# Optimization experiments

Hardware: AMD Instinct MI355X
Metric: run time of the kernel (lower is better)

The kernel has to match this reference:

```python
import jax, jax.numpy as jnp
import numpy as np

B, T, IN = 32, 1024, 256
H = 128          # hidden_size
NL = 2           # num_layers
NC = 4           # num_classes
F2 = 2 * H       # bidirectional feature size


def _lstm_dir(xs, w_ih, w_hh, b_ih, b_hh, reverse):
    # xs: [T, B, in]; w_ih: [4H, in]; w_hh: [4H, H]
    if reverse:
        xs = xs[::-1]
    h0 = jnp.zeros((xs.shape[1], H), xs.dtype)
    c0 = jnp.zeros((xs.shape[1], H), xs.dtype)

    def step(carry, xt):
        h, c = carry
        g = xt @ w_ih.T + b_ih + h @ w_hh.T + b_hh  # [B, 4H]
        i, f, gg, o = jnp.split(g, 4, axis=-1)       # PyTorch gate order i,f,g,o
        c = jax.nn.sigmoid(f) * c + jax.nn.sigmoid(i) * jnp.tanh(gg)
        h = jax.nn.sigmoid(o) * jnp.tanh(c)
        return (h, c), h

    _, hs = jax.lax.scan(step, (h0, c0), xs)  # [T, B, H]
    if reverse:
        hs = hs[::-1]
    return hs


def setup_inputs() -> dict:
    key = jax.random.key(0)
    ks = jax.random.split(key, 12)
    s = 0.05
    x = jax.random.normal(ks[0], (B, T, IN), jnp.float32)
    # stacked LSTM params: [layer, direction, ...]; layer0 in = IN, layer1 in = 2H = IN
    w_ih = jax.random.normal(ks[1], (NL, 2, 4 * H, IN), jnp.float32) * s
    w_hh = jax.random.normal(ks[2], (NL, 2, 4 * H, H), jnp.float32) * s
    b_ih = jax.random.normal(ks[3], (NL, 2, 4 * H), jnp.float32) * s
    b_hh = jax.random.normal(ks[4], (NL, 2, 4 * H), jnp.float32) * s
    wq = jax.random.normal(ks[5], (F2, F2), jnp.float32) * s
    wk = jax.random.normal(ks[6], (F2, F2), jnp.float32) * s
    wv = jax.random.normal(ks[7], (F2, F2), jnp.float32) * s
    bq = jax.random.normal(ks[8], (F2,), jnp.float32) * s
    bk = jax.random.normal(ks[9], (F2,), jnp.float32) * s
    bv = jax.random.normal(ks[10], (F2,), jnp.float32) * s
    w_fc = jax.random.normal(ks[11], (NC, F2), jnp.float32) * s
    b_fc = jnp.zeros((NC,), jnp.float32)
    return {"x": x, "w_ih": w_ih, "w_hh": w_hh, "b_ih": b_ih, "b_hh": b_hh,
            "wq": wq, "wk": wk, "wv": wv, "bq": bq, "bk": bk, "bv": bv,
            "w_fc": w_fc, "b_fc": b_fc}


def reference(x, w_ih, w_hh, b_ih, b_hh, wq, wk, wv, bq, bk, bv, w_fc, b_fc):
    # --- biLSTM (eval mode: inter-layer dropout inactive) ---
    xs = jnp.swapaxes(x, 0, 1)  # time-major [T, B, IN]
    for l in range(NL):
        fwd = _lstm_dir(xs, w_ih[l, 0], w_hh[l, 0], b_ih[l, 0], b_hh[l, 0], False)
        bwd = _lstm_dir(xs, w_ih[l, 1], w_hh[l, 1], b_ih[l, 1], b_hh[l, 1], True)
        xs = jnp.concatenate([fwd, bwd], axis=-1)  # [T, B, 2H]
    out = jnp.swapaxes(xs, 0, 1)  # [B, T, 2H]
    # --- naive full self-attention ---
    q = out @ wq.T + bq
    k = out @ wk.T + bk
    v = out @ wv.T + bv
    scores = jnp.einsum('btd,bsd->bts', q, k) / jnp.sqrt(jnp.float32(F2))
    attn = jax.nn.softmax(scores, axis=-1)          # [B, T, T]
    ctx = jnp.einsum('bts,bsd->btd', attn, v)       # [B, T, 2H]
    # --- FC head on last timestep ---
    return ctx[:, -1, :] @ w_fc.T + b_fc            # [B, NC]
```

## Files before the change

### kernel.cpp

```cpp
#include <hip/hip_runtime.h>
#include <math.h>
#include <stdint.h>

#define BB 32
#define TT 1024
#define HH 128
#define G4 512
#define CH 16

typedef _Float16 half2_t __attribute__((ext_vector_type(2)));
typedef _Float16 half8_t __attribute__((ext_vector_type(8)));
typedef float f32x4 __attribute__((ext_vector_type(4)));

__device__ __forceinline__ float fdot2f(half2_t a, half2_t b, float c) {
    return __builtin_amdgcn_fdot2(a, b, c, false);
}
__device__ __forceinline__ float rcpf(float x) {
    return __builtin_amdgcn_rcpf(x);
}
__device__ __forceinline__ float dpp_xor1(float x) {
    return __builtin_bit_cast(float, __builtin_amdgcn_update_dpp(
        0, __builtin_bit_cast(int, x), 0xB1, 0xF, 0xF, true));
}
__device__ __forceinline__ float dpp_xor2(float x) {
    return __builtin_bit_cast(float, __builtin_amdgcn_update_dpp(
        0, __builtin_bit_cast(int, x), 0x4E, 0xF, 0xF, true));
}
__device__ __forceinline__ void bar_lgkm() {
    asm volatile("s_waitcnt lgkmcnt(0)\n\ts_barrier" ::: "memory");
}

__global__ __launch_bounds__(256) void cvt_wih(
    const float* __restrict__ w, _Float16* __restrict__ o)
{
    const int i = (blockIdx.x * 256 + threadIdx.x) * 4;
    float4 f = *(const float4*)(w + i);
    half2_t t[2] = { half2_t{(_Float16)f.x, (_Float16)f.y},
                     half2_t{(_Float16)f.z, (_Float16)f.w} };
    *(float2*)(o + i) = *(float2*)t;
}

__global__ __launch_bounds__(512, 1) void lstm_fused(
    const float* __restrict__ x_in,
    const _Float16* __restrict__ wih16_l,
    const float* __restrict__ b_ih_l,
    const float* __restrict__ b_hh_l,
    const float* __restrict__ w_hh_l,
    float* __restrict__ out)
{
    const int b = blockIdx.x & 31;
    const int d = blockIdx.x >> 5;
    const int tid = threadIdx.x;
    const int wvid = tid >> 6;
    const int l = tid & 63;
    const int s = l & 3;
    const int g = l >> 2;
    const int j = (wvid << 4) | g;

    __shared__ __align__(16) _Float16 hs[HH];
    __shared__ __align__(16) float xp[2][CH * 512];
    __shared__ __align__(16) half2_t xr[2][CH * 128];
    __shared__ __align__(16) float obuf[CH * HH];

    half2_t wv[4][16];
#pragma unroll
    for (int G = 0; G < 4; ++G) {
        const float* wr = w_hh_l + (size_t)(d * G4 + 128 * G + j) * HH + 32 * s;
#pragma unroll
        for (int q4 = 0; q4 < 8; ++q4) {
            float4 f = *(const float4*)(wr + 4 * q4);
            wv[G][2 * q4]     = half2_t{(_Float16)f.x, (_Float16)f.y};
            wv[G][2 * q4 + 1] = half2_t{(_Float16)f.z, (_Float16)f.w};
        }
    }

    const int acol0 = wvid * 64 + (l & 15);
    const _Float16* wn = wih16_l + ((size_t)d * G4 + acol0) * 256 + (l >> 4) * 8;
    const float bias0 = b_ih_l[d * G4 + acol0]      + b_hh_l[d * G4 + acol0];
    const float bias1 = b_ih_l[d * G4 + acol0 + 16] + b_hh_l[d * G4 + acol0 + 16];
    const float bias2 = b_ih_l[d * G4 + acol0 + 32] + b_hh_l[d * G4 + acol0 + 32];
    const float bias3 = b_ih_l[d * G4 + acol0 + 48] + b_hh_l[d * G4 + acol0 + 48];

    const float* xbase = x_in + (size_t)b * TT * 256;

    const int a_noswz = (l & 15) * 512 + (l >> 4) * 16;
    const int a_swz   = (l & 7) << 4;
    const int w_swz_byte = (tid * 16) ^ (((tid >> 5) & 7) << 4);

#pragma unroll 1
    for (int p = 0; p < 2; ++p) {
        const int tlo = d ? (1008 - p * CH) : p * CH;
        const float* gs = xbase + (size_t)tlo * 256 + tid * 8;
        float4 f0 = *(const float4*)gs;
        float4 f1 = *(const float4*)(gs + 4);
        half2_t t4[4] = { half2_t{(_Float16)f0.x, (_Float16)f0.y},
                          half2_t{(_Float16)f0.z, (_Float16)f0.w},
                          half2_t{(_Float16)f1.x, (_Float16)f1.y},
                          half2_t{(_Float16)f1.z, (_Float16)f1.w} };
        *(float4*)((char*)xr[p] + w_swz_byte) = *(float4*)t4;
    }
    __syncthreads();

    f32x4 acc0 = {bias0, bias0, bias0, bias0};
    f32x4 acc1 = {bias1, bias1, bias1, bias1};
    f32x4 acc2 = {bias2, bias2, bias2, bias2};
    f32x4 acc3 = {bias3, bias3, bias3, bias3};

#pragma unroll
    for (int kt = 0; kt < 8; ++kt) {
        half8_t af = *(const half8_t*)((const char*)xr[0] + ((a_noswz + kt * 64) ^ a_swz));
        acc0 = __builtin_amdgcn_mfma_f32_16x16x32_f16(af, *(const half8_t*)(wn +         kt * 32), acc0, 0, 0, 0);
        acc1 = __builtin_amdgcn_mfma_f32_16x16x32_f16(af, *(const half8_t*)(wn +  4096 + kt * 32), acc1, 0, 0, 0);
        acc2 = __builtin_amdgcn_mfma_f32_16x16x32_f16(af, *(const half8_t*)(wn +  8192 + kt * 32), acc2, 0, 0, 0);
        acc3 = __builtin_amdgcn_mfma_f32_16x16x32_f16(af, *(const half8_t*)(wn + 12288 + kt * 32), acc3, 0, 0, 0);
    }
    {
        const int rb = (l >> 4) * 4;
#pragma unroll
        for (int q = 0; q < 4; ++q) {
            xp[0][(rb + q) * 512 + acol0]      = acc0[q];
            xp[0][(rb + q) * 512 + acol0 + 16] = acc1[q];
            xp[0][(rb + q) * 512 + acol0 + 32] = acc2[q];
            xp[0][(rb + q) * 512 + acol0 + 48] = acc3[q];
        }
    }
    acc0 = (f32x4){bias0, bias0, bias0, bias0};
    acc1 = (f32x4){bias1, bias1, bias1, bias1};
    acc2 = (f32x4){bias2, bias2, bias2, bias2};
    acc3 = (f32x4){bias3, bias3, bias3, bias3};

    if (tid < 64) ((half2_t*)hs)[tid] = half2_t{(_Float16)0.f, (_Float16)0.f};
    float c = 0.f;
    float* ob = out + (size_t)b * TT * 256 + d * HH;
    __syncthreads();

    float4 rg0 = {}, rg1 = {};
    half8_t afrag = {};
    for (int ck = 0; ck < 64; ++ck) {
        const int cur = ck & 1;
        const bool doproj = (ck + 1 < 64);
        if (ck + 2 < 64) {
            const int tlo2 = d ? (1008 - (ck + 2) * CH) : (ck + 2) * CH;
            const float* gs = xbase + (size_t)tlo2 * 256 + tid * 8;
            rg0 = *(const float4*)gs;
            rg1 = *(const float4*)(gs + 4);
        }
        const float* xb = xp[cur];
        const char* xr_rd = (const char*)xr[cur ^ 1];

#pragma unroll 1
        for (int si = 0; si < CH; ++si) {
            half8_t bA = {}, bB = {};
            if (doproj) {
                const int kt = si >> 1;
                if (!(si & 1)) {
                    afrag = *(const half8_t*)(xr_rd + ((a_noswz + kt * 64) ^ a_swz));
                    bA = *(const half8_t*)(wn +        kt * 32);
                    bB = *(const half8_t*)(wn + 4096 + kt * 32);
                } else {
                    bA = *(const half8_t*)(wn +  8192 + kt * 32);
                    bB = *(const half8_t*)(wn + 12288 + kt * 32);
                }
            }

            const int lds_t = d ? (CH - 1 - si) : si;

            const float xi = xb[lds_t * 512 +       j];
            const float xf = xb[lds_t * 512 + 128 + j];
            const float xg = xb[lds_t * 512 + 256 + j];
            const float xo = xb[lds_t * 512 + 384 + j];

            const float4* hp = (const float4*)(hs + 32 * s);
            float4 hA = hp[0], hB = hp[1], hC = hp[2], hD = hp[3];
            half2_t hh[16];
            hh[0]  = __builtin_bit_cast(half2_t, hA.x);
            hh[1]  = __builtin_bit_cast(half2_t, hA.y);
            hh[2]  = __builtin_bit_cast(half2_t, hA.z);
            hh[3]  = __builtin_bit_cast(half2_t, hA.w);
            hh[4]  = __builtin_bit_cast(half2_t, hB.x);
            hh[5]  = __builtin_bit_cast(half2_t, hB.y);
            hh[6]  = __builtin_bit_cast(half2_t, hB.z);
            hh[7]  = __builtin_bit_cast(half2_t, hB.w);
            hh[8]  = __builtin_bit_cast(half2_t, hC.x);
            hh[9]  = __builtin_bit_cast(half2_t, hC.y);
            hh[10] = __builtin_bit_cast(half2_t, hC.z);
            hh[11] = __builtin_bit_cast(half2_t, hC.w);
            hh[12] = __builtin_bit_cast(half2_t, hD.x);
            hh[13] = __builtin_bit_cast(half2_t, hD.y);
            hh[14] = __builtin_bit_cast(half2_t, hD.z);
            hh[15] = __builtin_bit_cast(half2_t, hD.w);

            float a0 = 0.f, a1 = 0.f, a2 = 0.f, a3 = 0.f;
            float e0 = 0.f, e1 = 0.f, e2 = 0.f, e3 = 0.f;
#pragma unroll
            for (int kk = 0; kk < 8; ++kk) {
                a0 = fdot2f(wv[0][kk], hh[kk], a0);
                a1 = fdot2f(wv[1][kk], hh[kk], a1);
                a2 = fdot2f(wv[2][kk], hh[kk], a2);
                a3 = fdot2f(wv[3][kk], hh[kk], a3);
                e0 = fdot2f(wv[0][kk + 8], hh[kk + 8], e0);
                e1 = fdot2f(wv[1][kk + 8], hh[kk + 8], e1);
                e2 = fdot2f(wv[2][kk + 8], hh[kk + 8], e2);
                e3 = fdot2f(wv[3][kk + 8], hh[kk + 8], e3);
            }
            a0 += e0; a1 += e1; a2 += e2; a3 += e3;

            a0 += dpp_xor1(a0); a0 += dpp_xor2(a0);
            a1 += dpp_xor1(a1); a1 += dpp_xor2(a1);
            a2 += dpp_xor1(a2); a2 += dpp_xor2(a2);
            a3 += dpp_xor1(a3); a3 += dpp_xor2(a3);

            const float gi = rcpf(1.f + __expf(-(a0 + xi)));
            const float gf = rcpf(1.f + __expf(-(a1 + xf)));
            const float gg = 1.f - 2.f * rcpf(1.f + __expf(2.f * (a2 + xg)));
            const float go = rcpf(1.f + __expf(-(a3 + xo)));
            c = gf * c + gi * gg;
            const float th = 1.f - 2.f * rcpf(1.f + __expf(2.f * c));
            const float h = go * th;
            if (s == 0) {
                hs[j] = (_Float16)h;
                obuf[si * HH + j] = h;
            }

            if (doproj) {
                if (!(si & 1)) {
                    acc0 = __builtin_amdgcn_mfma_f32_16x16x32_f16(afrag, bA, acc0, 0, 0, 0);
                    acc1 = __builtin_amdgcn_mfma_f32_16x16x32_f16(afrag, bB, acc1, 0, 0, 0);
                } else {
                    acc2 = __builtin_amdgcn_mfma_f32_16x16x32_f16(afrag, bA, acc2, 0, 0, 0);
                    acc3 = __builtin_amdgcn_mfma_f32_16x16x32_f16(afrag, bB, acc3, 0, 0, 0);
                }
            }

            bar_lgkm();
        }

        {
            const int idx = tid * 4;
            const int sf = idx >> 7, jf = idx & 127;
            const int sg = ck * CH + sf;
            const int t  = d ? (TT - 1 - sg) : sg;
            float4 o0 = *(const float4*)&obuf[idx];
            *(float4*)&ob[(size_t)t * 256 + jf] = o0;
        }
        if (doproj) {
            float* xpn = xp[cur ^ 1];
            const int rb = (l >> 4) * 4;
#pragma unroll
            for (int q = 0; q < 4; ++q) {
                xpn[(rb + q) * 512 + acol0]      = acc0[q];
                xpn[(rb + q) * 512 + acol0 + 16] = acc1[q];
                xpn[(rb + q) * 512 + acol0 + 32] = acc2[q];
                xpn[(rb + q) * 512 + acol0 + 48] = acc3[q];
            }
            acc0 = (f32x4){bias0, bias0, bias0, bias0};
            acc1 = (f32x4){bias1, bias1, bias1, bias1};
            acc2 = (f32x4){bias2, bias2, bias2, bias2};
            acc3 = (f32x4){bias3, bias3, bias3, bias3};
        }
        if (ck + 2 < 64) {
            half2_t t4[4] = { half2_t{(_Float16)rg0.x, (_Float16)rg0.y},
                              half2_t{(_Float16)rg0.z, (_Float16)rg0.w},
                              half2_t{(_Float16)rg1.x, (_Float16)rg1.y},
                              half2_t{(_Float16)rg1.z, (_Float16)rg1.w} };
            *(float4*)((char*)xr[cur] + w_swz_byte) = *(float4*)t4;
        }
        __syncthreads();
    }
}

__global__ __launch_bounds__(256) void attn_kernel(
    const float* __restrict__ out1,
    const float* __restrict__ wq, const float* __restrict__ bq,
    const float* __restrict__ wk,
    const float* __restrict__ wv, const float* __restrict__ bv,
    const float* __restrict__ wfc, const float* __restrict__ bfc,
    float* __restrict__ outp)
{
    const int b = blockIdx.x;
    const int tid = threadIdx.x;
    __shared__ float xl[256], q[256], u[256], cx[256];
    __shared__ __align__(16) float r[256];
    __shared__ float sc[TT];
    __shared__ float red[256];

    const float* ob = out1 + (size_t)b * TT * 256;

    xl[tid] = ob[(size_t)(TT - 1) * 256 + tid];
    __syncthreads();

    float acc = bq[tid];
    const float* wqr = wq + (size_t)tid * 256;
#pragma unroll 4
    for (int k = 0; k < 256; ++k) acc += xl[k] * wqr[k];
    q[tid] = acc;
    __syncthreads();

    acc = 0.f;
#pragma unroll 4
    for (int dd = 0; dd < 256; ++dd) acc += q[dd] * wk[(size_t)dd * 256 + tid];
    r[tid] = acc;
    __syncthreads();

    const int wave = tid >> 6, lane = tid & 63;
    float4 r4 = *(const float4*)&r[lane * 4];
    for (int t = wave; t < TT; t += 4) {
        float4 o4 = *(const float4*)(ob + (size_t)t * 256 + lane * 4);
        float p = r4.x * o4.x + r4.y * o4.y + r4.z * o4.z + r4.w * o4.w;
#pragma unroll
        for (int off = 32; off > 0; off >>= 1) p += __shfl_down(p, off, 64);
        if (lane == 0) sc[t] = p * 0.0625f;
    }
    __syncthreads();

    float mx = -1e30f;
#pragma unroll
    for (int i = 0; i < 4; ++i) mx = fmaxf(mx, sc[tid + 256 * i]);
    red[tid] = mx; __syncthreads();
    for (int st = 128; st > 0; st >>= 1) {
        if (tid < st) red[tid] = fmaxf(red[tid], red[tid + st]);
        __syncthreads();
    }
    mx = red[0]; __syncthreads();
    float lsum = 0.f;
#pragma unroll
    for (int i = 0; i < 4; ++i) {
        float e = expf(sc[tid + 256 * i] - mx);
        sc[tid + 256 * i] = e;
        lsum += e;
    }
    __syncthreads();
    red[tid] = lsum; __syncthreads();
    for (int st = 128; st > 0; st >>= 1) {
        if (tid < st) red[tid] += red[tid + st];
        __syncthreads();
    }
    const float inv = 1.f / red[0];
    __syncthreads();

    acc = 0.f;
#pragma unroll 8
    for (int t = 0; t < TT; ++t) acc += sc[t] * ob[(size_t)t * 256 + tid];
    u[tid] = acc * inv;
    __syncthreads();

    acc = bv[tid];
#pragma unroll 4
    for (int k = 0; k < 256; ++k) acc += u[k] * wv[(size_t)tid * 256 + k];
    cx[tid] = acc;
    __syncthreads();

    if (tid < 4) {
        float o = bfc[tid];
        for (int k = 0; k < 256; ++k) o += cx[k] * wfc[tid * 256 + k];
        outp[b * 4 + tid] = o;
    }
}

extern "C" void kernel_launch(void* const* d_in, const int* in_sizes, int n_in,
                              void* d_out, int out_size, void* d_ws, size_t ws_size,
                              hipStream_t stream)
{
    const float* x    = (const float*)d_in[0];
    const float* w_ih = (const float*)d_in[1];
    const float* w_hh = (const float*)d_in[2];
    const float* b_ih = (const float*)d_in[3];
    const float* b_hh = (const float*)d_in[4];
    const float* wq   = (const float*)d_in[5];
    const float* wk   = (const float*)d_in[6];
    const float* wv   = (const float*)d_in[7];
    const float* bq   = (const float*)d_in[8];
    const float* bv   = (const float*)d_in[10];
    const float* wfc  = (const float*)d_in[11];
    const float* bfcv = (const float*)d_in[12];
    float* outp = (float*)d_out;

    float* ws = (float*)d_ws;
    _Float16* wih16 = (_Float16*)ws;
    float* out0 = ws + 262144;
    float* out1 = out0 + 8388608;

    cvt_wih<<<512, 256, 0, stream>>>(w_ih, wih16);

    lstm_fused<<<64, 512, 0, stream>>>(x, wih16, b_ih, b_hh, w_hh, out0);
    lstm_fused<<<64, 512, 0, stream>>>(out0, wih16 + 262144, b_ih + 1024, b_hh + 1024,
                                       w_hh + 2 * 512 * 128, out1);
    attn_kernel<<<32, 256, 0, stream>>>(out1, wq, bq, wk, wv, bv, wfc, bfcv, outp);
}
```

Before: 1.853 ms.

## Pad xp rows, prefetch MFMA operands a step ahead, widen attention block

Pads the per-timestep gate-preactivation rows in LDS from 512 to 514 floats to spread bank accesses. Loads the input-projection MFMA operands one recurrence step ahead so their latency is hidden behind the gate math. Separately, the attention kernel moves to 1024 threads per block, splitting each matvec and the weighted sum over time into four partial sums that are then reduced. This adds registers in the recurrent loop and extra syncs in attention.

```diff
diff --git a/kernel.cpp b/kernel.cpp
--- a/kernel.cpp
+++ b/kernel.cpp
@@ -7,6 +7,7 @@
 #define HH 128
 #define G4 512
 #define CH 16
+#define XPS 514
 
 typedef _Float16 half2_t __attribute__((ext_vector_type(2)));
 typedef _Float16 half8_t __attribute__((ext_vector_type(8)));
@@ -58,7 +59,7 @@
     const int j = (wvid << 4) | g;
 
     __shared__ __align__(16) _Float16 hs[HH];
-    __shared__ __align__(16) float xp[2][CH * 512];
+    __shared__ __align__(16) float xp[2][CH * XPS];
     __shared__ __align__(16) half2_t xr[2][CH * 128];
     __shared__ __align__(16) float obuf[CH * HH];
 
@@ -118,10 +119,10 @@
         const int rb = (l >> 4) * 4;
 #pragma unroll
         for (int q = 0; q < 4; ++q) {
-            xp[0][(rb + q) * 512 + acol0]      = acc0[q];
-            xp[0][(rb + q) * 512 + acol0 + 16] = acc1[q];
-            xp[0][(rb + q) * 512 + acol0 + 32] = acc2[q];
-            xp[0][(rb + q) * 512 + acol0 + 48] = acc3[q];
+            xp[0][(rb + q) * XPS + acol0]      = acc0[q];
+            xp[0][(rb + q) * XPS + acol0 + 16] = acc1[q];
+            xp[0][(rb + q) * XPS + acol0 + 32] = acc2[q];
+            xp[0][(rb + q) * XPS + acol0 + 48] = acc3[q];
         }
     }
     acc0 = (f32x4){bias0, bias0, bias0, bias0};
@@ -135,7 +136,6 @@
     __syncthreads();
 
     float4 rg0 = {}, rg1 = {};
-    half8_t afrag = {};
     for (int ck = 0; ck < 64; ++ck) {
         const int cur = ck & 1;
         const bool doproj = (ck + 1 < 64);
@@ -148,27 +148,34 @@
         const float* xb = xp[cur];
         const char* xr_rd = (const char*)xr[cur ^ 1];
 
+        half8_t fAf = {}, fA = {}, fB = {};
+        if (doproj) {
+            fAf = *(const half8_t*)(xr_rd + (a_noswz ^ a_swz));
+            fA  = *(const half8_t*)(wn);
+            fB  = *(const half8_t*)(wn + 4096);
+        }
+
 #pragma unroll 1
         for (int si = 0; si < CH; ++si) {
-            half8_t bA = {}, bB = {};
-            if (doproj) {
-                const int kt = si >> 1;
-                if (!(si & 1)) {
-                    afrag = *(const half8_t*)(xr_rd + ((a_noswz + kt * 64) ^ a_swz));
-                    bA = *(const half8_t*)(wn +        kt * 32);
-                    bB = *(const half8_t*)(wn + 4096 + kt * 32);
+            half8_t nAf = fAf, nA = {}, nB = {};
+            if (doproj && si < CH - 1) {
+                const int sn = si + 1, ktn = sn >> 1;
+                if (!(sn & 1)) {
+                    nAf = *(const half8_t*)(xr_rd + ((a_noswz + ktn * 64) ^ a_swz));
+                    nA  = *(const half8_t*)(wn +        ktn * 32);
+                    nB  = *(const half8_t*)(wn + 4096 + ktn * 32);
                 } else {
-                    bA = *(const half8_t*)(wn +  8192 + kt * 32);
-                    bB = *(const half8_t*)(wn + 12288 + kt * 32);
+                    nA  = *(const half8_t*)(wn +  8192 + ktn * 32);
+                    nB  = *(const half8_t*)(wn + 12288 + ktn * 32);
                 }
             }
 
             const int lds_t = d ? (CH - 1 - si) : si;
 
-            const float xi = xb[lds_t * 512 +       j];
-            const float xf = xb[lds_t * 512 + 128 + j];
-            const float xg = xb[lds_t * 512 + 256 + j];
-            const float xo = xb[lds_t * 512 + 384 + j];
+            const float xi = xb[lds_t * XPS +       j];
+            const float xf = xb[lds_t * XPS + 128 + j];
+            const float xg = xb[lds_t * XPS + 256 + j];
+            const float xo = xb[lds_t * XPS + 384 + j];
 
             const float4* hp = (const float4*)(hs + 32 * s);
             float4 hA = hp[0], hB = hp[1], hC = hp[2], hD = hp[3];
@@ -224,13 +231,14 @@
 
             if (doproj) {
                 if (!(si & 1)) {
-                    acc0 = __builtin_amdgcn_mfma_f32_16x16x32_f16(afrag, bA, acc0, 0, 0, 0);
-                    acc1 = __builtin_amdgcn_mfma_f32_16x16x32_f16(afrag, bB, acc1, 0, 0, 0);
+                    acc0 = __builtin_amdgcn_mfma_f32_16x16x32_f16(fAf, fA, acc0, 0, 0, 0);
+                    acc1 = __builtin_amdgcn_mfma_f32_16x16x32_f16(fAf, fB, acc1, 0, 0, 0);
                 } else {
-                    acc2 = __builtin_amdgcn_mfma_f32_16x16x32_f16(afrag, bA, acc2, 0, 0, 0);
-                    acc3 = __builtin_amdgcn_mfma_f32_16x16x32_f16(afrag, bB, acc3, 0, 0, 0);
+                    acc2 = __builtin_amdgcn_mfma_f32_16x16x32_f16(fAf, fA, acc2, 0, 0, 0);
+                    acc3 = __builtin_amdgcn_mfma_f32_16x16x32_f16(fAf, fB, acc3, 0, 0, 0);
                 }
             }
+            fAf = nAf; fA = nA; fB = nB;
 
             bar_lgkm();
         }
@@ -248,10 +256,10 @@
             const int rb = (l >> 4) * 4;
 #pragma unroll
             for (int q = 0; q < 4; ++q) {
-                xpn[(rb + q) * 512 + acol0]      = acc0[q];
-                xpn[(rb + q) * 512 + acol0 + 16] = acc1[q];
-                xpn[(rb + q) * 512 + acol0 + 32] = acc2[q];
-                xpn[(rb + q) * 512 + acol0 + 48] = acc3[q];
+                xpn[(rb + q) * XPS + acol0]      = acc0[q];
+                xpn[(rb + q) * XPS + acol0 + 16] = acc1[q];
+                xpn[(rb + q) * XPS + acol0 + 32] = acc2[q];
+                xpn[(rb + q) * XPS + acol0 + 48] = acc3[q];
             }
             acc0 = (f32x4){bias0, bias0, bias0, bias0};
             acc1 = (f32x4){bias1, bias1, bias1, bias1};
@@ -269,7 +277,7 @@
     }
 }
 
-__global__ __launch_bounds__(256) void attn_kernel(
+__global__ __launch_bounds__(1024) void attn_kernel(
     const float* __restrict__ out1,
     const float* __restrict__ wq, const float* __restrict__ bq,
     const float* __restrict__ wk,
@@ -279,75 +287,93 @@
 {
     const int b = blockIdx.x;
     const int tid = threadIdx.x;
+    const int n = tid & 255, qq = tid >> 8;
+
     __shared__ float xl[256], q[256], u[256], cx[256];
     __shared__ __align__(16) float r[256];
     __shared__ float sc[TT];
-    __shared__ float red[256];
+    __shared__ float red[1024];
+    __shared__ float part[4][256];
 
     const float* ob = out1 + (size_t)b * TT * 256;
 
-    xl[tid] = ob[(size_t)(TT - 1) * 256 + tid];
-    __syncthreads();
-
-    float acc = bq[tid];
-    const float* wqr = wq + (size_t)tid * 256;
-#pragma unroll 4
-    for (int k = 0; k < 256; ++k) acc += xl[k] * wqr[k];
-    q[tid] = acc;
-    __syncthreads();
-
-    acc = 0.f;
-#pragma unroll 4
-    for (int dd = 0; dd < 256; ++dd) acc += q[dd] * wk[(size_t)dd * 256 + tid];
-    r[tid] = acc;
-    __syncthreads();
-
-    const int wave = tid >> 6, lane = tid & 63;
-    float4 r4 = *(const float4*)&r[lane * 4];
-    for (int t = wave; t < TT; t += 4) {
-        float4 o4 = *(const float4*)(ob + (size_t)t * 256 + lane * 4);
-        float p = r4.x * o4.x + r4.y * o4.y + r4.z * o4.z + r4.w * o4.w;
-#pragma unroll
-        for (int off = 32; off > 0; off >>= 1) p += __shfl_down(p, off, 64);
-        if (lane == 0) sc[t] = p * 0.0625f;
-    }
-    __syncthreads();
-
-    float mx = -1e30f;
-#pragma unroll
-    for (int i = 0; i < 4; ++i) mx = fmaxf(mx, sc[tid + 256 * i]);
-    red[tid] = mx; __syncthreads();
-    for (int st = 128; st > 0; st >>= 1) {
+    if (tid < 256) xl[tid] = ob[(size_t)(TT - 1) * 256 + tid];
+    __syncthreads();
+
+    {
+        float a = 0.f;
+        const float* wr = wq + (size_t)n * 256 + qq * 64;
+        const float* xq = xl + qq * 64;
+#pragma unroll 8
+        for (int k = 0; k < 64; ++k) a += xq[k] * wr[k];
+        part[qq][n] = a;
+    }
+    __syncthreads();
+    if (tid < 256) q[tid] = bq[tid] + part[0][tid] + part[1][tid] + part[2][tid] + part[3][tid];
+    __syncthreads();
+
+    {
+        float a = 0.f;
+        const float* wkp = wk + (size_t)(qq * 64) * 256 + n;
+#pragma unroll 8
+        for (int dd = 0; dd < 64; ++dd) a += q[qq * 64 + dd] * wkp[(size_t)dd * 256];
+        part[qq][n] = a;
+    }
+    __syncthreads();
+    if (tid < 256) r[tid] = part[0][tid] + part[1][tid] + part[2][tid] + part[3][tid];
+    __syncthreads();
+
+    {
+        const int wave = tid >> 6, lane = tid & 63;
+        float4 r4 = *(const float4*)&r[lane * 4];
+        for (int t = wave; t < TT; t += 16) {
+            float4 o4 = *(const float4*)(ob + (size_t)t * 256 + lane * 4);
+            float p = r4.x * o4.x + r4.y * o4.y + r4.z * o4.z + r4.w * o4.w;
+#pragma unroll
+            for (int off = 32; off > 0; off >>= 1) p += __shfl_down(p, off, 64);
+            if (lane == 0) sc[t] = p * 0.0625f;
+        }
+    }
+    __syncthreads();
+
+    float v = sc[tid];
+    red[tid] = v; __syncthreads();
+    for (int st = 512; st > 0; st >>= 1) {
         if (tid < st) red[tid] = fmaxf(red[tid], red[tid + st]);
         __syncthreads();
     }
-    mx = red[0]; __syncthreads();
-    float lsum = 0.f;
-#pragma unroll
-    for (int i = 0; i < 4; ++i) {
-        float e = expf(sc[tid + 256 * i] - mx);
-        sc[tid + 256 * i] = e;
-        lsum += e;
-    }
-    __syncthreads();
-    red[tid] = lsum; __syncthreads();
-    for (int st = 128; st > 0; st >>= 1) {
+    const float mx = red[0]; __syncthreads();
+    const float e = expf(v - mx);
+    sc[tid] = e;
+    red[tid] = e; __syncthreads();
+    for (int st = 512; st > 0; st >>= 1) {
         if (tid < st) red[tid] += red[tid + st];
         __syncthreads();
     }
     const float inv = 1.f / red[0];
     __syncthreads();
 
-    acc = 0.f;
+    {
+        float a = 0.f;
+        const float* op = ob + (size_t)(qq * 256) * 256 + n;
+        const float* sp = sc + qq * 256;
+#pragma unroll 4
+        for (int t = 0; t < 256; ++t) a += sp[t] * op[(size_t)t * 256];
+        part[qq][n] = a;
+    }
+    __syncthreads();
+    if (tid < 256) u[tid] = (part[0][tid] + part[1][tid] + part[2][tid] + part[3][tid]) * inv;
+    __syncthreads();
+
+    {
+        float a = 0.f;
+        const float* wr = wv + (size_t)n * 256 + qq * 64;
 #pragma unroll 8
-    for (int t = 0; t < TT; ++t) acc += sc[t] * ob[(size_t)t * 256 + tid];
-    u[tid] = acc * inv;
-    __syncthreads();
-
-    acc = bv[tid];
-#pragma unroll 4
-    for (int k = 0; k < 256; ++k) acc += u[k] * wv[(size_t)tid * 256 + k];
-    cx[tid] = acc;
+        for (int k = 0; k < 64; ++k) a += u[qq * 64 + k] * wr[k];
+        part[qq][n] = a;
+    }
+    __syncthreads();
+    if (tid < 256) cx[tid] = bv[tid] + part[0][tid] + part[1][tid] + part[2][tid] + part[3][tid];
     __syncthreads();
 
     if (tid < 4) {
@@ -385,5 +411,5 @@
     lstm_fused<<<64, 512, 0, stream>>>(x, wih16, b_ih, b_hh, w_hh, out0);
     lstm_fused<<<64, 512, 0, stream>>>(out0, wih16 + 262144, b_ih + 1024, b_hh + 1024,
                                        w_hh + 2 * 512 * 128, out1);
-    attn_kernel<<<32, 256, 0, stream>>>(out1, wq, bq, wk, wv, bv, wfc, bfcv, outp);
-}
+    attn_kernel<<<32, 1024, 0, stream>>>(out1, wq, bq, wk, wv, bv, wfc, bfcv, outp);
+}
```

New measurement: 1.857 ms. Within noise of the previous version (+0.2%).
